# Kernel tuning notes

Hardware: AMD Instinct MI355X
Metric: run time of the kernel (lower is better)

Reference implementation:

```python
import jax, jax.numpy as jnp
import numpy as np

EP = 1e-4
MAX_ITER = 100
NEG = -1e9
H = 8


def _layernorm(x, g, b, eps=1e-5):
    m = jnp.mean(x, axis=-1, keepdims=True)
    v = jnp.mean((x - m) ** 2, axis=-1, keepdims=True)
    return (x - m) * jax.lax.rsqrt(v + eps) * g + b


def _nonsat(x):
    # Fixed-point iteration y_{n+1} = (2 y^3/3 + x)/(y^2 + 1); torch detaches y each
    # step, so gradient only flows through x in the final update.
    xs = jax.lax.stop_gradient(x)

    def step(y):
        y2 = y * y
        return (2.0 * y * y2 / 3.0 + xs) / (y2 + 1.0)

    def cond(st):
        y, yn, i = st
        return jnp.logical_and(jnp.mean(jnp.abs(yn - y)) > EP, i <= MAX_ITER)

    def body(st):
        y, yn, i = st
        return (yn, step(yn), i + 1)

    y_prev, _, _ = jax.lax.while_loop(cond, body, (xs, step(xs), jnp.int32(0)))
    y2 = y_prev * y_prev
    return (2.0 * y_prev * y2 / 3.0 + x) / (y2 + 1.0)


def setup_inputs() -> dict:
    key = jax.random.key(0)
    ks = jax.random.split(key, 20)
    S, B, E = 256, 64, 512
    DH, SW, DSS, DFF, DEPTH = 512, 64, 128, 2048, 32
    sd = 0.02
    inp = {
        'x_in': jax.random.normal(ks[0], (S, B, E), jnp.float32),
        'stack_prev': jax.random.normal(ks[1], (B, S, DEPTH, SW), jnp.float32),
        'k_mask': jnp.zeros((B, S), jnp.bool_),
        'ln1_g': jnp.ones((E,), jnp.float32),
        'ln1_b': jnp.zeros((E,), jnp.float32),
        'in_proj_w': jax.random.normal(ks[2], (E, 3 * E), jnp.float32) * sd,
        'in_proj_b': jnp.zeros((3 * E,), jnp.float32),
        'out_w': jax.random.normal(ks[3], (E, E), jnp.float32) * sd,
        'out_b': jnp.zeros((E,), jnp.float32),
        'W_w': jax.random.normal(ks[4], (E, DH), jnp.float32) * sd,
        'W_b': jnp.zeros((DH,), jnp.float32),
        'P_w': jax.random.normal(ks[5], (SW, DH), jnp.float32) * sd,
        'P_b': jnp.zeros((DH,), jnp.float32),
        'V_w': jax.random.normal(ks[6], (E + DH, DSS), jnp.float32) * sd,
        'U_w': jax.random.normal(ks[7], (DSS, E), jnp.float32) * sd,
        'A_w': jax.random.normal(ks[8], (DH, 3), jnp.float32) * sd,
        'A_b': jnp.zeros((3,), jnp.float32),
        'D_w': jax.random.normal(ks[9], (DH, SW), jnp.float32) * sd,
        'D_b': jnp.zeros((SW,), jnp.float32),
        'ln2_g': jnp.ones((E,), jnp.float32),
        'ln2_b': jnp.zeros((E,), jnp.float32),
        'ff1_w': jax.random.normal(ks[10], (E, DFF), jnp.float32) * sd,
        'ff1_b': jnp.zeros((DFF,), jnp.float32),
        'ff2_w': jax.random.normal(ks[11], (DFF, E), jnp.float32) * sd,
        'ff2_b': jnp.zeros((E,), jnp.float32),
    }
    return inp


def reference(x_in, stack_prev, k_mask, ln1_g, ln1_b, in_proj_w, in_proj_b, out_w,
              out_b, W_w, W_b, P_w, P_b, V_w, U_w, A_w, A_b, D_w, D_b, ln2_g,
              ln2_b, ff1_w, ff1_b, ff2_w, ff2_b):
    S, B, E = x_in.shape
    hd = E // H
    scale = 1.0 / np.sqrt(hd)

    # --- sublayer 0: pre-norm causal self-attention ---
    xn = _layernorm(x_in, ln1_g, ln1_b)
    qkv = xn @ in_proj_w + in_proj_b            # (S,B,3E)
    q, k, v = jnp.split(qkv, 3, axis=-1)
    q = q.reshape(S, B, H, hd)
    k = k.reshape(S, B, H, hd)
    v = v.reshape(S, B, H, hd)
    scores = jnp.einsum('sbhd,tbhd->bhst', q, k) * scale
    causal = jnp.triu(jnp.full((S, S), NEG, x_in.dtype), k=1)
    scores = scores + causal
    scores = jnp.where(k_mask[:, None, None, :], NEG, scores)
    attn = jax.nn.softmax(scores, axis=-1)
    ao = jnp.einsum('bhst,tbhd->sbhd', attn, v).reshape(S, B, E)
    x = x_in + ao @ out_w + out_b

    # --- stack-augmented memory ---
    stack_x = stack_prev[:, :, 0, :]            # (B,S,SW) top of stack
    xb = jnp.transpose(x, (1, 0, 2))            # (B,S,E)
    hidden = _nonsat(xb @ W_w + W_b + stack_x @ P_w + P_b)  # (B,S,DH)
    vx = jnp.concatenate([x, jnp.transpose(hidden, (1, 0, 2))], axis=-1)
    y = jax.nn.softmax(vx @ V_w, axis=-1) @ U_w
    x = jnp.maximum(x, y)

    stack_inp = _nonsat(hidden @ D_w + D_b)[:, :, None, :]   # (B,S,1,SW)
    ctrl = jax.nn.softmax(hidden @ A_w + A_b, axis=-1)[..., None, None]  # (B,S,3,1,1)
    zeros = jnp.zeros_like(stack_prev[:, :, :1])
    stack_down = jnp.concatenate([stack_prev[:, :, 1:], zeros], axis=2)
    stack_up = jnp.concatenate([stack_inp, stack_prev[:, :, :-1]], axis=2)
    stack = ctrl[:, :, 2] * stack_prev + ctrl[:, :, 0] * stack_up + ctrl[:, :, 1] * stack_down

    # --- sublayer 1: pre-norm FFN ---
    xn2 = _layernorm(x, ln2_g, ln2_b)
    x = x + jax.nn.relu(xn2 @ ff1_w + ff1_b) @ ff2_w + ff2_b
    return (x, stack)
```

## Files before the change

kernel.cpp:

```cpp
#include <hip/hip_runtime.h>
#include <math.h>

#define S_DIM 256
#define B_DIM 64
#define E_DIM 512
#define H_NUM 8
#define HD 64
#define DH 512
#define SW 64
#define DSS 128
#define DFF 2048
#define DEPTH 32
#define M_ROWS 16384

typedef __attribute__((ext_vector_type(8))) short bf16x8;
typedef __attribute__((ext_vector_type(4))) float f32x4;

__device__ __forceinline__ ushort f2bf(float v){
    unsigned int u = __float_as_uint(v);
    u += 0x7fffu + ((u >> 16) & 1u);
    return (ushort)(u >> 16);
}
__device__ __forceinline__ float bf2f(ushort s){
    return __uint_as_float(((unsigned int)s) << 16);
}
__device__ __forceinline__ void splitbf(float v, ushort& h, ushort& l){
    h = f2bf(v);
    l = f2bf(v - bf2f(h));
}

__device__ __forceinline__ float nonsat_f(float x){
    float y = x;
#pragma unroll
    for (int i = 0; i < 10; i++){
        float y2 = y * y;
        y = (0.66666666f * y * y2 + x) / (y2 + 1.0f);
    }
    return y;
}

__global__ __launch_bounds__(256) void ln_split(const float* __restrict__ x,
                                                const float* __restrict__ g,
                                                const float* __restrict__ bta,
                                                ushort* __restrict__ oh,
                                                ushort* __restrict__ ol){
    __shared__ float red[4];
    int r = blockIdx.x;
    int t = threadIdx.x;
    const float* xr = x + (size_t)r * E_DIM;
    float v0 = xr[t], v1 = xr[t + 256];
    float s = v0 + v1;
#pragma unroll
    for (int off = 32; off > 0; off >>= 1) s += __shfl_xor(s, off, 64);
    if ((t & 63) == 0) red[t >> 6] = s;
    __syncthreads();
    float mean = (red[0] + red[1] + red[2] + red[3]) * (1.0f / 512.0f);
    __syncthreads();
    float d0 = v0 - mean, d1 = v1 - mean;
    float q = d0 * d0 + d1 * d1;
#pragma unroll
    for (int off = 32; off > 0; off >>= 1) q += __shfl_xor(q, off, 64);
    if ((t & 63) == 0) red[t >> 6] = q;
    __syncthreads();
    float var = (red[0] + red[1] + red[2] + red[3]) * (1.0f / 512.0f);
    float rs = rsqrtf(var + 1e-5f);
    size_t base = (size_t)r * E_DIM;
    float y0 = d0 * rs * g[t]       + bta[t];
    float y1 = d1 * rs * g[t + 256] + bta[t + 256];
    ushort h, l;
    splitbf(y0, h, l); oh[base + t] = h;       ol[base + t] = l;
    splitbf(y1, h, l); oh[base + t + 256] = h; ol[base + t + 256] = l;
}

__global__ __launch_bounds__(256) void wsplit_t(const float* __restrict__ W,
                                                ushort* __restrict__ th,
                                                ushort* __restrict__ tl,
                                                int K, int N, int Ktot, int koff){
    __shared__ float tile[32][33];
    int n0 = blockIdx.x << 5, k0 = blockIdx.y << 5;
    int tx = threadIdx.x & 31, ty = threadIdx.x >> 5;
#pragma unroll
    for (int i = 0; i < 32; i += 8)
        tile[ty + i][tx] = W[(size_t)(k0 + ty + i) * N + (n0 + tx)];
    __syncthreads();
#pragma unroll
    for (int i = 0; i < 32; i += 8){
        int n = ty + i;
        float v = tile[tx][n];
        ushort h, l; splitbf(v, h, l);
        th[(size_t)(n0 + n) * Ktot + koff + k0 + tx] = h;
        tl[(size_t)(n0 + n) * Ktot + koff + k0 + tx] = l;
    }
}

__global__ __launch_bounds__(256) void build_dab(const float* __restrict__ Dw,
                                                 const float* __restrict__ Db,
                                                 const float* __restrict__ Aw,
                                                 const float* __restrict__ Ab,
                                                 const float* __restrict__ Wb,
                                                 const float* __restrict__ Pb,
                                                 float* __restrict__ DA,
                                                 float* __restrict__ dabb,
                                                 float* __restrict__ hbias){
    int idx = blockIdx.x * 256 + threadIdx.x;
    if (idx < 65536){
        int k = idx >> 7, c = idx & 127;
        float v = 0.f;
        if (c < 64) v = Dw[k * 64 + c];
        else if (c < 67) v = Aw[k * 3 + (c - 64)];
        DA[idx] = v;
    }
    if (idx < 128){
        float v = 0.f;
        if (idx < 64) v = Db[idx];
        else if (idx < 67) v = Ab[idx - 64];
        dabb[idx] = v;
    }
    if (idx < 512) hbias[idx] = Wb[idx] + Pb[idx];
}

__global__ __launch_bounds__(256) void gemm_bf3(
    const ushort* __restrict__ Ah, const ushort* __restrict__ Al,
    const ushort* __restrict__ Bh, const ushort* __restrict__ Bl,
    const float* __restrict__ bias, const float* __restrict__ res,
    float* __restrict__ Cf, ushort* __restrict__ Ch, ushort* __restrict__ Cl,
    int M, int N, int K, int act, int resmode)
{
    __shared__ ushort lds[16384];
    const int tid = threadIdx.x;
    const int n0 = blockIdx.x << 7, m0 = blockIdx.y << 7;

    const int srow = tid >> 2, schunk = tid & 3;
    const int sOff = srow * 32 + (((srow + schunk) & 3) << 3);
    const ushort* gA0 = Ah + (size_t)(m0 + srow) * K + (schunk << 3);
    const ushort* gA1 = Al + (size_t)(m0 + srow) * K + (schunk << 3);
    const ushort* gB0 = Bh + (size_t)(n0 + srow) * K + (schunk << 3);
    const ushort* gB1 = Bl + (size_t)(n0 + srow) * K + (schunk << 3);
    const size_t rstep = (size_t)64 * K;

    const int lane = tid & 63;
    const int wv = tid >> 6;
    const int wm = (wv >> 1) << 6, wn = (wv & 1) << 6;
    const int r0 = lane & 15, gq = lane >> 4;
    const int gsub = (gq & 1) << 2;
    const int gc = gq >> 1;

    f32x4 acc[4][4];
    f32x4 zero = {0.f, 0.f, 0.f, 0.f};
#pragma unroll
    for (int i = 0; i < 4; i++)
#pragma unroll
        for (int j = 0; j < 4; j++) acc[i][j] = zero;

    uint4 v0,v1,v2,v3,v4,v5,v6,v7;
    v0 = *(const uint4*)(gA0);          v1 = *(const uint4*)(gA0 + rstep);
    v2 = *(const uint4*)(gA1);          v3 = *(const uint4*)(gA1 + rstep);
    v4 = *(const uint4*)(gB0);          v5 = *(const uint4*)(gB0 + rstep);
    v6 = *(const uint4*)(gB1);          v7 = *(const uint4*)(gB1 + rstep);

    for (int k0 = 0; k0 < K; k0 += 32){
        __syncthreads();
        *(uint4*)(&lds[sOff])               = v0;
        *(uint4*)(&lds[sOff + 2048])        = v1;
        *(uint4*)(&lds[4096 + sOff])        = v2;
        *(uint4*)(&lds[4096 + sOff + 2048]) = v3;
        *(uint4*)(&lds[8192 + sOff])        = v4;
        *(uint4*)(&lds[8192 + sOff + 2048]) = v5;
        *(uint4*)(&lds[12288 + sOff])        = v6;
        *(uint4*)(&lds[12288 + sOff + 2048]) = v7;
        __syncthreads();
        if (k0 + 32 < K){
            gA0 += 32; gA1 += 32; gB0 += 32; gB1 += 32;
            v0 = *(const uint4*)(gA0);  v1 = *(const uint4*)(gA0 + rstep);
            v2 = *(const uint4*)(gA1);  v3 = *(const uint4*)(gA1 + rstep);
            v4 = *(const uint4*)(gB0);  v5 = *(const uint4*)(gB0 + rstep);
            v6 = *(const uint4*)(gB1);  v7 = *(const uint4*)(gB1 + rstep);
        }
        bf16x8 fa[4], fal[4];
#pragma unroll
        for (int fr = 0; fr < 4; fr++){
            int R = wm + (fr << 4) + r0;
            int base = R * 32 + gsub;
            int c0 = ((gc + R) & 3) << 3;
            int c1 = ((gc + 2 + R) & 3) << 3;
            uint2 p0 = *(const uint2*)(&lds[base + c0]);
            uint2 p1 = *(const uint2*)(&lds[base + c1]);
            union { unsigned int u[4]; bf16x8 v; } t0;
            t0.u[0] = p0.x; t0.u[1] = p0.y; t0.u[2] = p1.x; t0.u[3] = p1.y;
            fa[fr] = t0.v;
            uint2 q0 = *(const uint2*)(&lds[4096 + base + c0]);
            uint2 q1 = *(const uint2*)(&lds[4096 + base + c1]);
            union { unsigned int u[4]; bf16x8 v; } t1;
            t1.u[0] = q0.x; t1.u[1] = q0.y; t1.u[2] = q1.x; t1.u[3] = q1.y;
            fal[fr] = t1.v;
        }
#pragma unroll
        for (int fc = 0; fc < 4; fc++){
            int R = wn + (fc << 4) + r0;
            int base = R * 32 + gsub;
            int c0 = ((gc + R) & 3) << 3;
            int c1 = ((gc + 2 + R) & 3) << 3;
            uint2 p0 = *(const uint2*)(&lds[8192 + base + c0]);
            uint2 p1 = *(const uint2*)(&lds[8192 + base + c1]);
            union { unsigned int u[4]; bf16x8 v; } t0;
            t0.u[0] = p0.x; t0.u[1] = p0.y; t0.u[2] = p1.x; t0.u[3] = p1.y;
            bf16x8 fbh = t0.v;
            uint2 q0 = *(const uint2*)(&lds[12288 + base + c0]);
            uint2 q1 = *(const uint2*)(&lds[12288 + base + c1]);
            union { unsigned int u[4]; bf16x8 v; } t1;
            t1.u[0] = q0.x; t1.u[1] = q0.y; t1.u[2] = q1.x; t1.u[3] = q1.y;
            bf16x8 fbl = t1.v;
#pragma unroll
            for (int fr = 0; fr < 4; fr++){
                acc[fr][fc] = __builtin_amdgcn_mfma_f32_16x16x32_bf16(fa[fr],  fbh, acc[fr][fc], 0, 0, 0);
                acc[fr][fc] = __builtin_amdgcn_mfma_f32_16x16x32_bf16(fa[fr],  fbl, acc[fr][fc], 0, 0, 0);
                acc[fr][fc] = __builtin_amdgcn_mfma_f32_16x16x32_bf16(fal[fr], fbh, acc[fr][fc], 0, 0, 0);
            }
        }
    }
#pragma unroll
    for (int fc = 0; fc < 4; fc++){
        int col = n0 + wn + (fc << 4) + r0;
        float bc = bias ? bias[col] : 0.f;
#pragma unroll
        for (int fr = 0; fr < 4; fr++){
#pragma unroll
            for (int e = 0; e < 4; e++){
                int row = m0 + wm + (fr << 4) + (gq << 2) + e;
                size_t idx = (size_t)row * N + col;
                float v = acc[fr][fc][e] + bc;
                if (resmode == 1) v += res[idx];
                else if (resmode == 2) v = fmaxf(v, res[idx]);
                if (act == 1) v = fmaxf(v, 0.f);
                else if (act == 2) v = nonsat_f(v);
                if (Cf) Cf[idx] = v;
                if (Ch){ ushort hh, ll; splitbf(v, hh, ll); Ch[idx] = hh; Cl[idx] = ll; }
            }
        }
    }
}

__global__ __launch_bounds__(256) void gemm_hidden_bf3(
    const ushort* __restrict__ x1h, const ushort* __restrict__ x1l,
    const float* __restrict__ stack_prev,
    const ushort* __restrict__ Bh, const ushort* __restrict__ Bl,
    const float* __restrict__ bias,
    float* __restrict__ hidden)
{
    __shared__ ushort lds[16384];
    const int tid = threadIdx.x;
    const int n0 = blockIdx.x << 7, m0 = blockIdx.y << 7;
    const int srow = tid >> 2, schunk = tid & 3;
    const int sOff = srow * 32 + (((srow + schunk) & 3) << 3);
    const int ra = m0 + srow, rb = m0 + 64 + srow;
    const int xra = ((ra & 255) << 6) | (ra >> 8);
    const int xrb = ((rb & 255) << 6) | (rb >> 8);
    const ushort* gB0 = Bh + (size_t)(n0 + srow) * 576 + (schunk << 3);
    const ushort* gB1 = Bl + (size_t)(n0 + srow) * 576 + (schunk << 3);
    const size_t rstepB = (size_t)64 * 576;

    const int lane = tid & 63;
    const int wv = tid >> 6;
    const int wm = (wv >> 1) << 6, wn = (wv & 1) << 6;
    const int r0 = lane & 15, gq = lane >> 4;
    const int gsub = (gq & 1) << 2;
    const int gc = gq >> 1;

    auto fetchA = [&](int k0, int row, int xr, uint4& vh, uint4& vl){
        if (k0 < 512){
            vh = *(const uint4*)(x1h + (size_t)xr * 512 + k0 + (schunk << 3));
            vl = *(const uint4*)(x1l + (size_t)xr * 512 + k0 + (schunk << 3));
        } else {
            const float* sp = stack_prev + (size_t)row * 2048 + (k0 - 512) + (schunk << 3);
            float f[8];
            *(float4*)(f)     = *(const float4*)(sp);
            *(float4*)(f + 4) = *(const float4*)(sp + 4);
            union { ushort us[8]; uint4 u4; } th, tl;
#pragma unroll
            for (int j = 0; j < 8; j++) splitbf(f[j], th.us[j], tl.us[j]);
            vh = th.u4; vl = tl.u4;
        }
    };

    f32x4 acc[4][4];
    f32x4 zero = {0.f, 0.f, 0.f, 0.f};
#pragma unroll
    for (int i = 0; i < 4; i++)
#pragma unroll
        for (int j = 0; j < 4; j++) acc[i][j] = zero;

    uint4 v0,v1,v2,v3,v4,v5,v6,v7;
    fetchA(0, ra, xra, v0, v2);
    fetchA(0, rb, xrb, v1, v3);
    v4 = *(const uint4*)(gB0); v5 = *(const uint4*)(gB0 + rstepB);
    v6 = *(const uint4*)(gB1); v7 = *(const uint4*)(gB1 + rstepB);

    for (int k0 = 0; k0 < 576; k0 += 32){
        __syncthreads();
        *(uint4*)(&lds[sOff])               = v0;
        *(uint4*)(&lds[sOff + 2048])        = v1;
        *(uint4*)(&lds[4096 + sOff])        = v2;
        *(uint4*)(&lds[4096 + sOff + 2048]) = v3;
        *(uint4*)(&lds[8192 + sOff])        = v4;
        *(uint4*)(&lds[8192 + sOff + 2048]) = v5;
        *(uint4*)(&lds[12288 + sOff])        = v6;
        *(uint4*)(&lds[12288 + sOff + 2048]) = v7;
        __syncthreads();
        if (k0 + 32 < 576){
            fetchA(k0 + 32, ra, xra, v0, v2);
            fetchA(k0 + 32, rb, xrb, v1, v3);
            gB0 += 32; gB1 += 32;
            v4 = *(const uint4*)(gB0); v5 = *(const uint4*)(gB0 + rstepB);
            v6 = *(const uint4*)(gB1); v7 = *(const uint4*)(gB1 + rstepB);
        }
        bf16x8 fa[4], fal[4];
#pragma unroll
        for (int fr = 0; fr < 4; fr++){
            int R = wm + (fr << 4) + r0;
            int base = R * 32 + gsub;
            int c0 = ((gc + R) & 3) << 3;
            int c1 = ((gc + 2 + R) & 3) << 3;
            uint2 p0 = *(const uint2*)(&lds[base + c0]);
            uint2 p1 = *(const uint2*)(&lds[base + c1]);
            union { unsigned int u[4]; bf16x8 v; } t0;
            t0.u[0] = p0.x; t0.u[1] = p0.y; t0.u[2] = p1.x; t0.u[3] = p1.y;
            fa[fr] = t0.v;
            uint2 q0 = *(const uint2*)(&lds[4096 + base + c0]);
            uint2 q1 = *(const uint2*)(&lds[4096 + base + c1]);
            union { unsigned int u[4]; bf16x8 v; } t1;
            t1.u[0] = q0.x; t1.u[1] = q0.y; t1.u[2] = q1.x; t1.u[3] = q1.y;
            fal[fr] = t1.v;
        }
#pragma unroll
        for (int fc = 0; fc < 4; fc++){
            int R = wn + (fc << 4) + r0;
            int base = R * 32 + gsub;
            int c0 = ((gc + R) & 3) << 3;
            int c1 = ((gc + 2 + R) & 3) << 3;
            uint2 p0 = *(const uint2*)(&lds[8192 + base + c0]);
            uint2 p1 = *(const uint2*)(&lds[8192 + base + c1]);
            union { unsigned int u[4]; bf16x8 v; } t0;
            t0.u[0] = p0.x; t0.u[1] = p0.y; t0.u[2] = p1.x; t0.u[3] = p1.y;
            bf16x8 fbh = t0.v;
            uint2 q0 = *(const uint2*)(&lds[12288 + base + c0]);
            uint2 q1 = *(const uint2*)(&lds[12288 + base + c1]);
            union { unsigned int u[4]; bf16x8 v; } t1;
            t1.u[0] = q0.x; t1.u[1] = q0.y; t1.u[2] = q1.x; t1.u[3] = q1.y;
            bf16x8 fbl = t1.v;
#pragma unroll
            for (int fr = 0; fr < 4; fr++){
                acc[fr][fc] = __builtin_amdgcn_mfma_f32_16x16x32_bf16(fa[fr],  fbh, acc[fr][fc], 0, 0, 0);
                acc[fr][fc] = __builtin_amdgcn_mfma_f32_16x16x32_bf16(fa[fr],  fbl, acc[fr][fc], 0, 0, 0);
                acc[fr][fc] = __builtin_amdgcn_mfma_f32_16x16x32_bf16(fal[fr], fbh, acc[fr][fc], 0, 0, 0);
            }
        }
    }
#pragma unroll
    for (int fc = 0; fc < 4; fc++){
        int col = n0 + wn + (fc << 4) + r0;
        float bc = bias[col];
#pragma unroll
        for (int fr = 0; fr < 4; fr++){
#pragma unroll
            for (int e = 0; e < 4; e++){
                int row = m0 + wm + (fr << 4) + (gq << 2) + e;
                hidden[(size_t)row * 512 + col] = nonsat_f(acc[fr][fc][e] + bc);
            }
        }
    }
}

__global__ __launch_bounds__(256) void gemm_k(const float* __restrict__ A,
                                              const float* __restrict__ W,
                                              const float* __restrict__ bias,
                                              const float* __restrict__ res,
                                              float* __restrict__ C,
                                              int M, int N, int K,
                                              int act, int resmode){
    __shared__ float As[32][68];
    __shared__ float Ws[32][68];
    int m0 = blockIdx.x << 6, n0 = blockIdx.y << 6;
    int tid = threadIdx.x;
    int tx = tid & 15, ty = tid >> 4;
    float acc[4][4] = {{0.f}};
    for (int k0 = 0; k0 < K; k0 += 32){
#pragma unroll
        for (int i = 0; i < 8; i++){
            int e = tid + (i << 8);
            int row = e >> 5, col = e & 31;
            As[col][row] = A[(size_t)(m0 + row) * K + (k0 + col)];
        }
#pragma unroll
        for (int i = 0; i < 8; i++){
            int e = tid + (i << 8);
            int kk = e >> 6, nn = e & 63;
            Ws[kk][nn] = W[(size_t)(k0 + kk) * N + (n0 + nn)];
        }
        __syncthreads();
#pragma unroll
        for (int kk = 0; kk < 32; kk++){
            float4 a = *(const float4*)(&As[kk][ty << 2]);
            float4 b = *(const float4*)(&Ws[kk][tx << 2]);
            float av[4] = {a.x, a.y, a.z, a.w};
            float bv[4] = {b.x, b.y, b.z, b.w};
#pragma unroll
            for (int i = 0; i < 4; i++)
#pragma unroll
                for (int j = 0; j < 4; j++) acc[i][j] = fmaf(av[i], bv[j], acc[i][j]);
        }
        __syncthreads();
    }
    int nbase = n0 + (tx << 2);
    float4 bv4 = make_float4(0.f, 0.f, 0.f, 0.f);
    if (bias) bv4 = *(const float4*)(bias + nbase);
#pragma unroll
    for (int i = 0; i < 4; i++){
        int mm = m0 + (ty << 2) + i;
        size_t idx = (size_t)mm * N + nbase;
        float v0 = acc[i][0] + bv4.x, v1 = acc[i][1] + bv4.y;
        float v2 = acc[i][2] + bv4.z, v3 = acc[i][3] + bv4.w;
        if (resmode == 1){
            float4 rv = *(const float4*)(res + idx);
            v0 += rv.x; v1 += rv.y; v2 += rv.z; v3 += rv.w;
        } else if (resmode == 2){
            float4 rv = *(const float4*)(res + idx);
            v0 = fmaxf(v0, rv.x); v1 = fmaxf(v1, rv.y);
            v2 = fmaxf(v2, rv.z); v3 = fmaxf(v3, rv.w);
        }
        if (act == 1){
            v0 = fmaxf(v0, 0.f); v1 = fmaxf(v1, 0.f);
            v2 = fmaxf(v2, 0.f); v3 = fmaxf(v3, 0.f);
        }
        *(float4*)(C + idx) = make_float4(v0, v1, v2, v3);
    }
}

__global__ __launch_bounds__(256) void gemm_vx(const float* __restrict__ x1,
                                               const float* __restrict__ hidden,
                                               const float* __restrict__ Vw,
                                               float* __restrict__ t){
    __shared__ float As[32][68];
    __shared__ float Ws[32][68];
    int m0 = blockIdx.x << 6, n0 = blockIdx.y << 6;
    int tid = threadIdx.x;
    int tx = tid & 15, ty = tid >> 4;
    float acc[4][4] = {{0.f}};
    for (int k0 = 0; k0 < 1024; k0 += 32){
        if (k0 < 512){
#pragma unroll
            for (int i = 0; i < 8; i++){
                int e = tid + (i << 8);
                int row = e >> 5, col = e & 31;
                As[col][row] = x1[(size_t)(m0 + row) * 512 + (k0 + col)];
            }
        } else {
#pragma unroll
            for (int i = 0; i < 8; i++){
                int e = tid + (i << 8);
                int row = e >> 5, col = e & 31;
                int r = m0 + row;
                int hr = ((r & 63) << 8) | (r >> 6);
                As[col][row] = hidden[(size_t)hr * 512 + (k0 - 512 + col)];
            }
        }
#pragma unroll
        for (int i = 0; i < 8; i++){
            int e = tid + (i << 8);
            int kk = e >> 6, nn = e & 63;
            Ws[kk][nn] = Vw[(size_t)(k0 + kk) * 128 + (n0 + nn)];
        }
        __syncthreads();
#pragma unroll
        for (int kk = 0; kk < 32; kk++){
            float4 a = *(const float4*)(&As[kk][ty << 2]);
            float4 b = *(const float4*)(&Ws[kk][tx << 2]);
            float av[4] = {a.x, a.y, a.z, a.w};
            float bv[4] = {b.x, b.y, b.z, b.w};
#pragma unroll
            for (int i = 0; i < 4; i++)
#pragma unroll
                for (int j = 0; j < 4; j++) acc[i][j] = fmaf(av[i], bv[j], acc[i][j]);
        }
        __syncthreads();
    }
    int nbase = n0 + (tx << 2);
#pragma unroll
    for (int i = 0; i < 4; i++){
        int mm = m0 + (ty << 2) + i;
        *(float4*)(t + (size_t)mm * 128 + nbase) =
            make_float4(acc[i][0], acc[i][1], acc[i][2], acc[i][3]);
    }
}

__global__ __launch_bounds__(128) void softmax128(float* __restrict__ t){
    __shared__ float red[2];
    int r = blockIdx.x, c = threadIdx.x;
    float v = t[(size_t)r * 128 + c];
    float m = v;
#pragma unroll
    for (int off = 32; off > 0; off >>= 1) m = fmaxf(m, __shfl_xor(m, off, 64));
    if ((c & 63) == 0) red[c >> 6] = m;
    __syncthreads();
    m = fmaxf(red[0], red[1]);
    __syncthreads();
    float e = expf(v - m);
    float s = e;
#pragma unroll
    for (int off = 32; off > 0; off >>= 1) s += __shfl_xor(s, off, 64);
    if ((c & 63) == 0) red[c >> 6] = s;
    __syncthreads();
    s = red[0] + red[1];
    t[(size_t)r * 128 + c] = e / s;
}

__global__ __launch_bounds__(256) void attn_kernel(const float* __restrict__ qkv,
                                                   ushort* __restrict__ aoh,
                                                   ushort* __restrict__ aol){
    __shared__ float Qs[64 * 68];
    __shared__ float KV[64 * 68];
    __shared__ float Ps[64 * 68];
    int bid = blockIdx.x;
    int ti = bid & 3, h = (bid >> 2) & 7, b = bid >> 5;
    int tid = threadIdx.x;
    int tx = tid & 15, ty = tid >> 4;
    const float scale = 0.125f;

    {
        const float* qbase = qkv + (size_t)b * 1536 + (h << 6);
#pragma unroll
        for (int i = 0; i < 4; i++){
            int f4 = tid + (i << 8);
            int r = f4 >> 4, c4 = f4 & 15;
            *(float4*)(&Qs[r * 68 + (c4 << 2)]) =
                *(const float4*)(qbase + (size_t)(((ti << 6) + r) << 6) * 1536 + (c4 << 2));
        }
    }
    float m_i[4], l_i[4], O[4][4];
#pragma unroll
    for (int i = 0; i < 4; i++){
        m_i[i] = -1e30f; l_i[i] = 0.f;
#pragma unroll
        for (int j = 0; j < 4; j++) O[i][j] = 0.f;
    }

    for (int tk = 0; tk <= ti; tk++){
        __syncthreads();
        {
            const float* kbase = qkv + (size_t)b * 1536 + 512 + (h << 6);
#pragma unroll
            for (int i = 0; i < 4; i++){
                int f4 = tid + (i << 8);
                int r = f4 >> 4, c4 = f4 & 15;
                *(float4*)(&KV[(r << 6) + (((c4 ^ (r >> 2)) & 15) << 2)]) =
                    *(const float4*)(kbase + (size_t)(((tk << 6) + r) << 6) * 1536 + (c4 << 2));
            }
        }
        __syncthreads();
        float sv[4][4] = {{0.f}};
#pragma unroll
        for (int d4 = 0; d4 < 16; d4++){
            float4 qa[4], kb[4];
#pragma unroll
            for (int i = 0; i < 4; i++)
                qa[i] = *(const float4*)(&Qs[((ty << 2) + i) * 68 + (d4 << 2)]);
#pragma unroll
            for (int j = 0; j < 4; j++)
                kb[j] = *(const float4*)(&KV[(((tx << 2) + j) << 6) + (((d4 ^ tx) & 15) << 2)]);
#pragma unroll
            for (int i = 0; i < 4; i++)
#pragma unroll
                for (int j = 0; j < 4; j++){
                    sv[i][j] = fmaf(qa[i].x, kb[j].x, sv[i][j]);
                    sv[i][j] = fmaf(qa[i].y, kb[j].y, sv[i][j]);
                    sv[i][j] = fmaf(qa[i].z, kb[j].z, sv[i][j]);
                    sv[i][j] = fmaf(qa[i].w, kb[j].w, sv[i][j]);
                }
        }
#pragma unroll
        for (int i = 0; i < 4; i++)
#pragma unroll
            for (int j = 0; j < 4; j++){
                float v = sv[i][j] * scale;
                if (tk == ti && ((tx << 2) + j) > ((ty << 2) + i)) v = -1e30f;
                sv[i][j] = v;
            }
        float alpha[4];
#pragma unroll
        for (int i = 0; i < 4; i++){
            float rm = fmaxf(fmaxf(sv[i][0], sv[i][1]), fmaxf(sv[i][2], sv[i][3]));
#pragma unroll
            for (int off = 8; off > 0; off >>= 1) rm = fmaxf(rm, __shfl_xor(rm, off, 64));
            float mn = fmaxf(m_i[i], rm);
            alpha[i] = __expf(m_i[i] - mn);
            float rs = 0.f;
#pragma unroll
            for (int j = 0; j < 4; j++){
                sv[i][j] = __expf(sv[i][j] - mn);
                rs += sv[i][j];
            }
#pragma unroll
            for (int off = 8; off > 0; off >>= 1) rs += __shfl_xor(rs, off, 64);
            l_i[i] = l_i[i] * alpha[i] + rs;
            m_i[i] = mn;
        }
#pragma unroll
        for (int i = 0; i < 4; i++)
            *(float4*)(&Ps[((ty << 2) + i) * 68 + (tx << 2)]) =
                make_float4(sv[i][0], sv[i][1], sv[i][2], sv[i][3]);
        __syncthreads();
        {
            const float* vbase = qkv + (size_t)b * 1536 + 1024 + (h << 6);
#pragma unroll
            for (int i = 0; i < 4; i++){
                int f4 = tid + (i << 8);
                int r = f4 >> 4, c4 = f4 & 15;
                *(float4*)(&KV[r * 68 + (c4 << 2)]) =
                    *(const float4*)(vbase + (size_t)(((tk << 6) + r) << 6) * 1536 + (c4 << 2));
            }
        }
        __syncthreads();
#pragma unroll
        for (int i = 0; i < 4; i++)
#pragma unroll
            for (int j = 0; j < 4; j++) O[i][j] *= alpha[i];
#pragma unroll
        for (int t4 = 0; t4 < 16; t4++){
            float4 pa[4], vb[4];
#pragma unroll
            for (int i = 0; i < 4; i++)
                pa[i] = *(const float4*)(&Ps[((ty << 2) + i) * 68 + (t4 << 2)]);
#pragma unroll
            for (int tt = 0; tt < 4; tt++)
                vb[tt] = *(const float4*)(&KV[((t4 << 2) + tt) * 68 + (tx << 2)]);
#pragma unroll
            for (int i = 0; i < 4; i++){
                float pav[4] = {pa[i].x, pa[i].y, pa[i].z, pa[i].w};
#pragma unroll
                for (int tt = 0; tt < 4; tt++){
                    O[i][0] = fmaf(pav[tt], vb[tt].x, O[i][0]);
                    O[i][1] = fmaf(pav[tt], vb[tt].y, O[i][1]);
                    O[i][2] = fmaf(pav[tt], vb[tt].z, O[i][2]);
                    O[i][3] = fmaf(pav[tt], vb[tt].w, O[i][3]);
                }
            }
        }
    }
#pragma unroll
    for (int i = 0; i < 4; i++){
        float inv = 1.0f / l_i[i];
        int sglob = (ti << 6) + (ty << 2) + i;
        size_t idx = (size_t)((sglob << 6) + b) * 512 + (h << 6) + (tx << 2);
        ushort4 hv, lv;
        float o0 = O[i][0] * inv, o1 = O[i][1] * inv, o2 = O[i][2] * inv, o3 = O[i][3] * inv;
        splitbf(o0, hv.x, lv.x);
        splitbf(o1, hv.y, lv.y);
        splitbf(o2, hv.z, lv.z);
        splitbf(o3, hv.w, lv.w);
        *(ushort4*)(aoh + idx) = hv;
        *(ushort4*)(aol + idx) = lv;
    }
}

__global__ __launch_bounds__(256) void stack_update(const float* __restrict__ head,
                                                    const float* __restrict__ stack_prev,
                                                    float* __restrict__ stack_out){
    __shared__ float sinp[64];
    __shared__ float ctrl[3];
    int r = blockIdx.x;
    int tid = threadIdx.x;
    const float* hrow = head + (size_t)r * 128;
    if (tid < 64){
        sinp[tid] = nonsat_f(hrow[tid]);
    } else if (tid == 64){
        float a0 = hrow[64], a1 = hrow[65], a2 = hrow[66];
        float mx = fmaxf(a0, fmaxf(a1, a2));
        float e0 = expf(a0 - mx), e1 = expf(a1 - mx), e2 = expf(a2 - mx);
        float inv = 1.f / (e0 + e1 + e2);
        ctrl[0] = e0 * inv; ctrl[1] = e1 * inv; ctrl[2] = e2 * inv;
    }
    __syncthreads();
    float c0 = ctrl[0], c1 = ctrl[1], c2 = ctrl[2];
    const float* prow = stack_prev + (size_t)r * 2048;
    float* orow = stack_out + (size_t)r * 2048;
#pragma unroll
    for (int i = 0; i < 8; i++){
        int idx = tid + (i << 8);
        int dep = idx >> 6, j = idx & 63;
        float prev = prow[idx];
        float up   = dep ? prow[idx - 64] : sinp[j];
        float down = (dep < 31) ? prow[idx + 64] : 0.f;
        orow[idx] = c2 * prev + c0 * up + c1 * down;
    }
}

extern "C" void kernel_launch(void* const* d_in, const int* in_sizes, int n_in,
                              void* d_out, int out_size, void* d_ws, size_t ws_size,
                              hipStream_t stream){
    const float* x_in       = (const float*)d_in[0];
    const float* stack_prev = (const float*)d_in[1];
    const float* ln1_g = (const float*)d_in[3];
    const float* ln1_b = (const float*)d_in[4];
    const float* in_proj_w = (const float*)d_in[5];
    const float* in_proj_b = (const float*)d_in[6];
    const float* out_w = (const float*)d_in[7];
    const float* out_b = (const float*)d_in[8];
    const float* W_w = (const float*)d_in[9];
    const float* W_b = (const float*)d_in[10];
    const float* P_w = (const float*)d_in[11];
    const float* P_b = (const float*)d_in[12];
    const float* V_w = (const float*)d_in[13];
    const float* U_w = (const float*)d_in[14];
    const float* A_w = (const float*)d_in[15];
    const float* A_b = (const float*)d_in[16];
    const float* D_w = (const float*)d_in[17];
    const float* D_b = (const float*)d_in[18];
    const float* ln2_g = (const float*)d_in[19];
    const float* ln2_b = (const float*)d_in[20];
    const float* ff1_w = (const float*)d_in[21];
    const float* ff1_b = (const float*)d_in[22];
    const float* ff2_w = (const float*)d_in[23];
    const float* ff2_b = (const float*)d_in[24];

    float* dout_x     = (float*)d_out;
    float* dout_stack = dout_x + 8388608;
    float* qkv = dout_stack;
    float* x1  = dout_stack + 25165824;
    ushort* x1h = (ushort*)dout_stack;
    ushort* x1l = x1h + 8388608;
    ushort* fmh = (ushort*)(dout_stack + 8388608);
    ushort* fml = fmh + 16777216;

    float* ws   = (float*)d_ws;
    float* bufA = ws;
    float* x2   = ws + 8388608;
    float* tbuf = ws + 16777216;
    ushort* xnh = (ushort*)(ws + 18874368);
    ushort* xnl = xnh + 8388608;
    ushort* wb0 = (ushort*)(ws + 27262976);
    ushort* ipTh = wb0;
    ushort* ipTl = ipTh + 786432;
    ushort* owTh = ipTl + 786432;
    ushort* owTl = owTh + 262144;
    ushort* f1Th = owTl + 262144;
    ushort* f1Tl = f1Th + 1048576;
    ushort* f2Th = f1Tl + 1048576;
    ushort* f2Tl = f2Th + 1048576;
    ushort* whT  = f2Tl + 1048576;
    ushort* wlT  = whT + 294912;
    float* headbuf = ws + 30703616;
    float* DAw   = ws + 32800768;
    float* dabb  = ws + 32866304;
    float* hbias = ws + 32866432;

    wsplit_t<<<dim3(48, 16), 256, 0, stream>>>(in_proj_w, ipTh, ipTl, 512, 1536, 512, 0);
    wsplit_t<<<dim3(16, 16), 256, 0, stream>>>(out_w, owTh, owTl, 512, 512, 512, 0);
    wsplit_t<<<dim3(64, 16), 256, 0, stream>>>(ff1_w, f1Th, f1Tl, 512, 2048, 512, 0);
    wsplit_t<<<dim3(16, 64), 256, 0, stream>>>(ff2_w, f2Th, f2Tl, 2048, 512, 2048, 0);
    wsplit_t<<<dim3(16, 16), 256, 0, stream>>>(W_w, whT, wlT, 512, 512, 576, 0);
    wsplit_t<<<dim3(16, 2), 256, 0, stream>>>(P_w, whT, wlT, 64, 512, 576, 512);
    build_dab<<<256, 256, 0, stream>>>(D_w, D_b, A_w, A_b, W_b, P_b, DAw, dabb, hbias);

    ln_split<<<16384, 256, 0, stream>>>(x_in, ln1_g, ln1_b, xnh, xnl);
    gemm_bf3<<<dim3(12, 128), 256, 0, stream>>>(xnh, xnl, ipTh, ipTl, in_proj_b, nullptr,
                                                qkv, nullptr, nullptr, 16384, 1536, 512, 0, 0);
    attn_kernel<<<2048, 256, 0, stream>>>(qkv, xnh, xnl);
    gemm_bf3<<<dim3(4, 128), 256, 0, stream>>>(xnh, xnl, owTh, owTl, out_b, x_in,
                                               x1, x1h, x1l, 16384, 512, 512, 0, 1);
    gemm_hidden_bf3<<<dim3(4, 128), 256, 0, stream>>>(x1h, x1l, stack_prev, whT, wlT,
                                                      hbias, bufA);
    gemm_k<<<dim3(256, 2), 256, 0, stream>>>(bufA, DAw, dabb, nullptr, headbuf,
                                             16384, 128, 512, 0, 0);
    gemm_vx<<<dim3(256, 2), 256, 0, stream>>>(x1, bufA, V_w, tbuf);
    softmax128<<<16384, 128, 0, stream>>>(tbuf);
    gemm_k<<<dim3(256, 8), 256, 0, stream>>>(tbuf, U_w, nullptr, x1, x2,
                                             16384, 512, 128, 0, 2);
    ln_split<<<16384, 256, 0, stream>>>(x2, ln2_g, ln2_b, xnh, xnl);
    for (int c = 0; c < 2; c++){
        gemm_bf3<<<dim3(16, 64), 256, 0, stream>>>(xnh + c * 4194304, xnl + c * 4194304,
                                                   f1Th, f1Tl, ff1_b, nullptr,
                                                   nullptr, fmh, fml, 8192, 2048, 512, 1, 0);
        gemm_bf3<<<dim3(4, 64), 256, 0, stream>>>(fmh, fml, f2Th, f2Tl, ff2_b,
                                                  x2 + c * 4194304, dout_x + c * 4194304,
                                                  nullptr, nullptr, 8192, 512, 2048, 0, 1);
    }
    stack_update<<<16384, 256, 0, stream>>>(headbuf, stack_prev, dout_stack);
}
```

Baseline: 1.512 ms.

## Permute K layout so MFMA fragments load as single 16-byte LDS reads

```diff
diff --git a/kernel.cpp b/kernel.cpp
--- a/kernel.cpp
+++ b/kernel.cpp
@@ -29,6 +29,10 @@
     l = f2bf(v - bf2f(h));
 }
 
+__device__ __forceinline__ int perm32(int k){
+    return ((k >> 2) & 3) * 8 + (k & 3) + ((k >> 4) << 2);
+}
+
 __device__ __forceinline__ float nonsat_f(float x){
     float y = x;
 #pragma unroll
@@ -67,9 +71,10 @@
     size_t base = (size_t)r * E_DIM;
     float y0 = d0 * rs * g[t]       + bta[t];
     float y1 = d1 * rs * g[t + 256] + bta[t + 256];
+    int pc = (t & ~31) | perm32(t & 31);
     ushort h, l;
-    splitbf(y0, h, l); oh[base + t] = h;       ol[base + t] = l;
-    splitbf(y1, h, l); oh[base + t + 256] = h; ol[base + t + 256] = l;
+    splitbf(y0, h, l); oh[base + pc] = h;       ol[base + pc] = l;
+    splitbf(y1, h, l); oh[base + pc + 256] = h; ol[base + pc + 256] = l;
 }
 
 __global__ __launch_bounds__(256) void wsplit_t(const float* __restrict__ W,
@@ -83,13 +88,14 @@
     for (int i = 0; i < 32; i += 8)
         tile[ty + i][tx] = W[(size_t)(k0 + ty + i) * N + (n0 + tx)];
     __syncthreads();
+    int pk = perm32(tx);
 #pragma unroll
     for (int i = 0; i < 32; i += 8){
         int n = ty + i;
         float v = tile[tx][n];
         ushort h, l; splitbf(v, h, l);
-        th[(size_t)(n0 + n) * Ktot + koff + k0 + tx] = h;
-        tl[(size_t)(n0 + n) * Ktot + koff + k0 + tx] = l;
+        th[(size_t)(n0 + n) * Ktot + koff + k0 + pk] = h;
+        tl[(size_t)(n0 + n) * Ktot + koff + k0 + pk] = l;
     }
 }
 
@@ -126,12 +132,15 @@
     float* __restrict__ Cf, ushort* __restrict__ Ch, ushort* __restrict__ Cl,
     int M, int N, int K, int act, int resmode)
 {
-    __shared__ ushort lds[16384];
+    __shared__ __align__(16) ushort lds[20480];
     const int tid = threadIdx.x;
-    const int n0 = blockIdx.x << 7, m0 = blockIdx.y << 7;
+    int lin = blockIdx.y * gridDim.x + blockIdx.x;
+    int nloc = (gridDim.x * gridDim.y) >> 3;
+    int id = (lin & 7) * nloc + (lin >> 3);
+    const int n0 = (id % gridDim.x) << 7, m0 = (id / gridDim.x) << 7;
 
     const int srow = tid >> 2, schunk = tid & 3;
-    const int sOff = srow * 32 + (((srow + schunk) & 3) << 3);
+    const int sOff = srow * 40 + (schunk << 3);
     const ushort* gA0 = Ah + (size_t)(m0 + srow) * K + (schunk << 3);
     const ushort* gA1 = Al + (size_t)(m0 + srow) * K + (schunk << 3);
     const ushort* gB0 = Bh + (size_t)(n0 + srow) * K + (schunk << 3);
@@ -142,8 +151,6 @@
     const int wv = tid >> 6;
     const int wm = (wv >> 1) << 6, wn = (wv & 1) << 6;
     const int r0 = lane & 15, gq = lane >> 4;
-    const int gsub = (gq & 1) << 2;
-    const int gc = gq >> 1;
 
     f32x4 acc[4][4];
     f32x4 zero = {0.f, 0.f, 0.f, 0.f};
@@ -160,14 +167,14 @@
 
     for (int k0 = 0; k0 < K; k0 += 32){
         __syncthreads();
-        *(uint4*)(&lds[sOff])               = v0;
-        *(uint4*)(&lds[sOff + 2048])        = v1;
-        *(uint4*)(&lds[4096 + sOff])        = v2;
-        *(uint4*)(&lds[4096 + sOff + 2048]) = v3;
-        *(uint4*)(&lds[8192 + sOff])        = v4;
-        *(uint4*)(&lds[8192 + sOff + 2048]) = v5;
-        *(uint4*)(&lds[12288 + sOff])        = v6;
-        *(uint4*)(&lds[12288 + sOff + 2048]) = v7;
+        *(uint4*)(&lds[sOff])                = v0;
+        *(uint4*)(&lds[sOff + 2560])         = v1;
+        *(uint4*)(&lds[5120 + sOff])         = v2;
+        *(uint4*)(&lds[5120 + sOff + 2560])  = v3;
+        *(uint4*)(&lds[10240 + sOff])        = v4;
+        *(uint4*)(&lds[10240 + sOff + 2560]) = v5;
+        *(uint4*)(&lds[15360 + sOff])        = v6;
+        *(uint4*)(&lds[15360 + sOff + 2560]) = v7;
         __syncthreads();
         if (k0 + 32 < K){
             gA0 += 32; gA1 += 32; gB0 += 32; gB1 += 32;
@@ -179,37 +186,15 @@
         bf16x8 fa[4], fal[4];
 #pragma unroll
         for (int fr = 0; fr < 4; fr++){
-            int R = wm + (fr << 4) + r0;
-            int base = R * 32 + gsub;
-            int c0 = ((gc + R) & 3) << 3;
-            int c1 = ((gc + 2 + R) & 3) << 3;
-            uint2 p0 = *(const uint2*)(&lds[base + c0]);
-            uint2 p1 = *(const uint2*)(&lds[base + c1]);
-            union { unsigned int u[4]; bf16x8 v; } t0;
-            t0.u[0] = p0.x; t0.u[1] = p0.y; t0.u[2] = p1.x; t0.u[3] = p1.y;
-            fa[fr] = t0.v;
-            uint2 q0 = *(const uint2*)(&lds[4096 + base + c0]);
-            uint2 q1 = *(const uint2*)(&lds[4096 + base + c1]);
-            union { unsigned int u[4]; bf16x8 v; } t1;
-            t1.u[0] = q0.x; t1.u[1] = q0.y; t1.u[2] = q1.x; t1.u[3] = q1.y;
-            fal[fr] = t1.v;
+            int off = (wm + (fr << 4) + r0) * 40 + (gq << 3);
+            fa[fr]  = *(const bf16x8*)(&lds[off]);
+            fal[fr] = *(const bf16x8*)(&lds[off + 5120]);
         }
 #pragma unroll
         for (int fc = 0; fc < 4; fc++){
-            int R = wn + (fc << 4) + r0;
-            int base = R * 32 + gsub;
-            int c0 = ((gc + R) & 3) << 3;
-            int c1 = ((gc + 2 + R) & 3) << 3;
-            uint2 p0 = *(const uint2*)(&lds[8192 + base + c0]);
-            uint2 p1 = *(const uint2*)(&lds[8192 + base + c1]);
-            union { unsigned int u[4]; bf16x8 v; } t0;
-            t0.u[0] = p0.x; t0.u[1] = p0.y; t0.u[2] = p1.x; t0.u[3] = p1.y;
-            bf16x8 fbh = t0.v;
-            uint2 q0 = *(const uint2*)(&lds[12288 + base + c0]);
-            uint2 q1 = *(const uint2*)(&lds[12288 + base + c1]);
-            union { unsigned int u[4]; bf16x8 v; } t1;
-            t1.u[0] = q0.x; t1.u[1] = q0.y; t1.u[2] = q1.x; t1.u[3] = q1.y;
-            bf16x8 fbl = t1.v;
+            int off = (wn + (fc << 4) + r0) * 40 + (gq << 3);
+            bf16x8 fbh = *(const bf16x8*)(&lds[off + 10240]);
+            bf16x8 fbl = *(const bf16x8*)(&lds[off + 15360]);
 #pragma unroll
             for (int fr = 0; fr < 4; fr++){
                 acc[fr][fc] = __builtin_amdgcn_mfma_f32_16x16x32_bf16(fa[fr],  fbh, acc[fr][fc], 0, 0, 0);
@@ -221,6 +206,7 @@
 #pragma unroll
     for (int fc = 0; fc < 4; fc++){
         int col = n0 + wn + (fc << 4) + r0;
+        int pcol = (col & ~31) | perm32(col & 31);
         float bc = bias ? bias[col] : 0.f;
 #pragma unroll
         for (int fr = 0; fr < 4; fr++){
@@ -234,7 +220,11 @@
                 if (act == 1) v = fmaxf(v, 0.f);
                 else if (act == 2) v = nonsat_f(v);
                 if (Cf) Cf[idx] = v;
-                if (Ch){ ushort hh, ll; splitbf(v, hh, ll); Ch[idx] = hh; Cl[idx] = ll; }
+                if (Ch){
+                    ushort hh, ll; splitbf(v, hh, ll);
+                    size_t pidx = (size_t)row * N + pcol;
+                    Ch[pidx] = hh; Cl[pidx] = ll;
+                }
             }
         }
     }
@@ -247,11 +237,15 @@
     const float* __restrict__ bias,
     float* __restrict__ hidden)
 {
-    __shared__ ushort lds[16384];
+    __shared__ __align__(16) ushort lds[20480];
     const int tid = threadIdx.x;
-    const int n0 = blockIdx.x << 7, m0 = blockIdx.y << 7;
+    int lin = blockIdx.y * gridDim.x + blockIdx.x;
+    int nloc = (gridDim.x * gridDim.y) >> 3;
+    int id = (lin & 7) * nloc + (lin >> 3);
+    const int n0 = (id % gridDim.x) << 7, m0 = (id / gridDim.x) << 7;
+
     const int srow = tid >> 2, schunk = tid & 3;
-    const int sOff = srow * 32 + (((srow + schunk) & 3) << 3);
+    const int sOff = srow * 40 + (schunk << 3);
     const int ra = m0 + srow, rb = m0 + 64 + srow;
     const int xra = ((ra & 255) << 6) | (ra >> 8);
     const int xrb = ((rb & 255) << 6) | (rb >> 8);
@@ -263,18 +257,16 @@
     const int wv = tid >> 6;
     const int wm = (wv >> 1) << 6, wn = (wv & 1) << 6;
     const int r0 = lane & 15, gq = lane >> 4;
-    const int gsub = (gq & 1) << 2;
-    const int gc = gq >> 1;
 
     auto fetchA = [&](int k0, int row, int xr, uint4& vh, uint4& vl){
         if (k0 < 512){
             vh = *(const uint4*)(x1h + (size_t)xr * 512 + k0 + (schunk << 3));
             vl = *(const uint4*)(x1l + (size_t)xr * 512 + k0 + (schunk << 3));
         } else {
-            const float* sp = stack_prev + (size_t)row * 2048 + (k0 - 512) + (schunk << 3);
+            const float* sp = stack_prev + (size_t)row * 2048 + (k0 - 512) + (schunk << 2);
             float f[8];
             *(float4*)(f)     = *(const float4*)(sp);
-            *(float4*)(f + 4) = *(const float4*)(sp + 4);
+            *(float4*)(f + 4) = *(const float4*)(sp + 16);
             union { ushort us[8]; uint4 u4; } th, tl;
 #pragma unroll
             for (int j = 0; j < 8; j++) splitbf(f[j], th.us[j], tl.us[j]);
@@ -297,14 +289,14 @@
 
     for (int k0 = 0; k0 < 576; k0 += 32){
         __syncthreads();
-        *(uint4*)(&lds[sOff])               = v0;
-        *(uint4*)(&lds[sOff + 2048])        = v1;
-        *(uint4*)(&lds[4096 + sOff])        = v2;
-        *(uint4*)(&lds[4096 + sOff + 2048]) = v3;
-        *(uint4*)(&lds[8192 + sOff])        = v4;
-        *(uint4*)(&lds[8192 + sOff + 2048]) = v5;
-        *(uint4*)(&lds[12288 + sOff])        = v6;
-        *(uint4*)(&lds[12288 + sOff + 2048]) = v7;
+        *(uint4*)(&lds[sOff])                = v0;
+        *(uint4*)(&lds[sOff + 2560])         = v1;
+        *(uint4*)(&lds[5120 + sOff])         = v2;
+        *(uint4*)(&lds[5120 + sOff + 2560])  = v3;
+        *(uint4*)(&lds[10240 + sOff])        = v4;
+        *(uint4*)(&lds[10240 + sOff + 2560]) = v5;
+        *(uint4*)(&lds[15360 + sOff])        = v6;
+        *(uint4*)(&lds[15360 + sOff + 2560]) = v7;
         __syncthreads();
         if (k0 + 32 < 576){
             fetchA(k0 + 32, ra, xra, v0, v2);
@@ -316,37 +308,15 @@
         bf16x8 fa[4], fal[4];
 #pragma unroll
         for (int fr = 0; fr < 4; fr++){
-            int R = wm + (fr << 4) + r0;
-            int base = R * 32 + gsub;
-            int c0 = ((gc + R) & 3) << 3;
-            int c1 = ((gc + 2 + R) & 3) << 3;
-            uint2 p0 = *(const uint2*)(&lds[base + c0]);
-            uint2 p1 = *(const uint2*)(&lds[base + c1]);
-            union { unsigned int u[4]; bf16x8 v; } t0;
-            t0.u[0] = p0.x; t0.u[1] = p0.y; t0.u[2] = p1.x; t0.u[3] = p1.y;
-            fa[fr] = t0.v;
-            uint2 q0 = *(const uint2*)(&lds[4096 + base + c0]);
-            uint2 q1 = *(const uint2*)(&lds[4096 + base + c1]);
-            union { unsigned int u[4]; bf16x8 v; } t1;
-            t1.u[0] = q0.x; t1.u[1] = q0.y; t1.u[2] = q1.x; t1.u[3] = q1.y;
-            fal[fr] = t1.v;
+            int off = (wm + (fr << 4) + r0) * 40 + (gq << 3);
+            fa[fr]  = *(const bf16x8*)(&lds[off]);
+            fal[fr] = *(const bf16x8*)(&lds[off + 5120]);
         }
 #pragma unroll
         for (int fc = 0; fc < 4; fc++){
-            int R = wn + (fc << 4) + r0;
-            int base = R * 32 + gsub;
-            int c0 = ((gc + R) & 3) << 3;
-            int c1 = ((gc + 2 + R) & 3) << 3;
-            uint2 p0 = *(const uint2*)(&lds[8192 + base + c0]);
-            uint2 p1 = *(const uint2*)(&lds[8192 + base + c1]);
-            union { unsigned int u[4]; bf16x8 v; } t0;
-            t0.u[0] = p0.x; t0.u[1] = p0.y; t0.u[2] = p1.x; t0.u[3] = p1.y;
-            bf16x8 fbh = t0.v;
-            uint2 q0 = *(const uint2*)(&lds[12288 + base + c0]);
-            uint2 q1 = *(const uint2*)(&lds[12288 + base + c1]);
-            union { unsigned int u[4]; bf16x8 v; } t1;
-            t1.u[0] = q0.x; t1.u[1] = q0.y; t1.u[2] = q1.x; t1.u[3] = q1.y;
-            bf16x8 fbl = t1.v;
+            int off = (wn + (fc << 4) + r0) * 40 + (gq << 3);
+            bf16x8 fbh = *(const bf16x8*)(&lds[off + 10240]);
+            bf16x8 fbl = *(const bf16x8*)(&lds[off + 15360]);
 #pragma unroll
             for (int fr = 0; fr < 4; fr++){
                 acc[fr][fc] = __builtin_amdgcn_mfma_f32_16x16x32_bf16(fa[fr],  fbh, acc[fr][fc], 0, 0, 0);
@@ -649,7 +619,9 @@
     for (int i = 0; i < 4; i++){
         float inv = 1.0f / l_i[i];
         int sglob = (ti << 6) + (ty << 2) + i;
-        size_t idx = (size_t)((sglob << 6) + b) * 512 + (h << 6) + (tx << 2);
+        int col = (h << 6) + (tx << 2);
+        int pcol = (col & ~31) | perm32(col & 31);
+        size_t idx = (size_t)((sglob << 6) + b) * 512 + pcol;
         ushort4 hv, lv;
         float o0 = O[i][0] * inv, o1 = O[i][1] * inv, o2 = O[i][2] * inv, o3 = O[i][3] * inv;
         splitbf(o0, hv.x, lv.x);
```

Result: faster. 1.358 ms (-10.2%).
